# Kernel tuning notes

Hardware: AMD Instinct MI355X
Metric: run time of the kernel (lower is better)

## Reference

```python
import jax, jax.numpy as jnp
import numpy as np

B, T, N = 16, 16, 1024          # patients, max visits, code_num
C, G, H, A, P = 48, 32, 150, 32, 32  # code_size, graph_size, hidden_size, t_attention_size, pool attn size
OUT = 1
NEG = -1e30


def setup_inputs() -> dict:
    key = jax.random.key(0)
    ks = jax.random.split(key, 20)
    code_x = (jax.random.uniform(ks[0], (B, T, N)) < 0.2).astype(jnp.float32)
    neighbors = (jax.random.uniform(ks[1], (B, T, N)) < 0.2).astype(jnp.float32)
    cat = jax.random.randint(ks[2], (B, T, N), 0, 8)
    # divided[..., 0/1/2] = disjoint m1 (persistent) / m2 (emerging-neighbor) / m3 (emerging-unrelated) masks
    divided = jnp.stack([(cat == 0), (cat == 1), (cat == 2)], axis=-1).astype(jnp.int32)
    lens = jax.random.randint(ks[3], (B,), 1, T + 1)
    prior = jax.random.uniform(ks[4], (N,))
    adj = (jax.random.uniform(ks[5], (N, N)) * (jax.random.uniform(ks[6], (N, N)) < 0.05)).astype(jnp.float32)

    def nrm(k, shape, scale=0.05):
        return (jax.random.normal(k, shape) * scale).astype(jnp.float32)

    return dict(
        code_x=code_x, divided=divided, neighbors=neighbors, lens=lens, prior=prior, adj=adj,
        c_emb=nrm(ks[7], (N, C)), n_emb=nrm(ks[8], (N, C)), u_emb=nrm(ks[9], (N, G)),
        Wg=nrm(ks[10], (C, G)), bg=jnp.zeros((G,), jnp.float32),
        W_ih=nrm(ks[11], (3 * H, G)), b_ih=jnp.zeros((3 * H,), jnp.float32),
        W_hh=nrm(ks[12], (3 * H, H)), b_hh=jnp.zeros((3 * H,), jnp.float32),
        Wq=nrm(ks[13], (G, A)), bq=jnp.zeros((A,), jnp.float32),
        Wk=nrm(ks[14], (G, A)), bk=jnp.zeros((A,), jnp.float32),
        Wv=nrm(ks[15], (G, H)), bv=jnp.zeros((H,), jnp.float32),
        Wp=nrm(ks[16], (H, P)), bp=jnp.zeros((P,), jnp.float32),
        ctx=nrm(ks[17], (P,)),
        Wc=nrm(ks[18], (H, OUT)), bc=jnp.zeros((OUT,), jnp.float32),
    )


def _forward(code_x, divided, neighbors, lens, prior, adj, c_emb, n_emb, u_emb,
             Wg, bg, W_ih, b_ih, W_hh, b_hh, Wq, bq, Wk, bk, Wv, bv,
             Wp, bp, ctx, Wc, bc):
    pr = prior[:, None]                                  # [N,1] disease prior scaling of graph messages
    scale = 1.0 / jnp.sqrt(jnp.asarray(A, jnp.float32))

    def gru(x, h):
        # torch nn.GRUCell semantics; x: [B,N,G], h: [B,N,H]
        gi = jnp.einsum('bng,kg->bnk', x, W_ih) + b_ih
        gh = jnp.einsum('bnh,kh->bnk', h, W_hh) + b_hh
        ir, iz, i_n = jnp.split(gi, 3, -1)
        hr, hz, h_n = jnp.split(gh, 3, -1)
        r = jax.nn.sigmoid(ir + hr)
        z = jax.nn.sigmoid(iz + hz)
        cand = jnp.tanh(i_n + r * h_n)
        return (1.0 - z) * cand + z * h

    def step(carry, xs):
        h_prev, no_prev, t = carry
        cx, nb, dv = xs                                  # [B,N], [B,N], [B,N,3]
        c = cx[..., None]
        n = nb[..., None]
        # --- GraphLayer: adjacency message passing, prior-weighted ---
        ce = c * c_emb                                   # [B,N,C]
        ne = n * n_emb
        agg_c = jnp.einsum('mn,bnc->bmc', adj, ce) * pr
        agg_n = jnp.einsum('mn,bnc->bmc', adj, ne) * pr
        co = jax.nn.leaky_relu((ce + c * (agg_c + agg_n)) @ Wg + bg)   # [B,N,G]
        no = jax.nn.leaky_relu((ne + n * (agg_n + agg_c)) @ Wg + bg)
        # --- TransitionLayer ---
        m1 = dv[..., 0] > 0
        m2 = dv[..., 1] > 0
        m3 = dv[..., 2] > 0
        m23 = m2 | m3
        h_gru = gru(co, h_prev)                          # GRU branch for persistent codes (m1)
        # attention branch: queries = prev-step neighbor embeddings (m2) or unrelated embeddings (m3)
        qf = jnp.where(m2[..., None], no_prev, 0.0) + jnp.where(m3[..., None], u_emb, 0.0)
        q = qf @ Wq + bq
        k = co @ Wk + bk
        v = co @ Wv + bv                                 # [B,N,H]
        g = jnp.einsum('bma,bna->bmn', q, k) * scale     # scores over active m2|m3 keys only
        g = jnp.where(m23[:, None, :], g, NEG)
        h_att = jnp.tanh(jnp.einsum('bmn,bnh->bmh', jax.nn.softmax(g, axis=-1), v))
        t_pos = (t > 0).astype(co.dtype)                 # m23 branch only runs for t > 0 (as in original)
        h_new = jnp.where(m1[..., None], h_gru, 0.0) + t_pos * jnp.where(m23[..., None], h_att, 0.0)
        # masked maxes (0 when the index set is empty, as in original)
        om1 = jnp.max(jnp.where(m1[..., None], h_gru, NEG), axis=1)
        om1 = jnp.where(jnp.any(m1, axis=1)[:, None], om1, 0.0)
        om23 = jnp.max(jnp.where(m23[..., None], h_att, NEG), axis=1)
        om23 = jnp.where(jnp.any(m23, axis=1)[:, None], om23, 0.0)
        out_t = om1 + t_pos * om23                       # [B,H]
        return (h_new, no, t + 1), out_t

    h0 = jnp.zeros((B, N, H), jnp.float32)
    no0 = jnp.zeros((B, N, G), jnp.float32)
    xs = (jnp.transpose(code_x, (1, 0, 2)),
          jnp.transpose(neighbors, (1, 0, 2)),
          jnp.transpose(divided, (1, 0, 2, 3)))
    _, outs = jax.lax.scan(step, (h0, no0, jnp.int32(0)), xs)
    outs = jnp.transpose(outs, (1, 0, 2))                # [B,T,H]
    # --- DotProductAttention pooling over valid (ragged) timesteps ---
    vu = (outs @ Wp + bp) @ ctx                          # [B,T]
    valid = jnp.arange(T)[None, :] < lens[:, None]
    score = jax.nn.softmax(jnp.where(valid, vu, NEG), axis=-1)
    pooled = jnp.sum(outs * score[..., None], axis=1)    # [B,H]
    # --- Classifier (dropout identity at eval, activation=None) ---
    return pooled @ Wc + bc


def reference(code_x, divided, neighbors, lens, prior, adj, c_emb, n_emb, u_emb,
              Wg, bg, W_ih, b_ih, W_hh, b_hh, Wq, bq, Wk, bk, Wv, bv,
              Wp, bp, ctx, Wc, bc):
    return _forward(code_x, divided, neighbors, lens, prior, adj, c_emb, n_emb, u_emb,
                    Wg, bg, W_ih, b_ih, W_hh, b_hh, Wq, bq, Wk, bk, Wv, bv,
                    Wp, bp, ctx, Wc, bc)
```

## Files before the change

kernel.cpp:

```cpp
#include <hip/hip_runtime.h>

#define B_ 16
#define T_ 16
#define N_ 1024
#define C_ 48
#define G_ 32
#define H_ 150
#define A_ 32
#define P_ 32
#define H3_ 450
#define NNZ_CAP 262144
#define CAP1 256
#define CAP23 384
#define CHCAP 40960
#define DCAP 256
#define SCALE_ 0.17677669529663687f

__device__ __forceinline__ unsigned fenc(float f){
  unsigned u = __float_as_uint(f);
  return (u & 0x80000000u) ? ~u : (u | 0x80000000u);
}
__device__ __forceinline__ float fdec(unsigned e){
  unsigned u = (e & 0x80000000u) ? (e & 0x7fffffffu) : ~e;
  return __uint_as_float(u);
}
__device__ __forceinline__ float sigmf(float x){ return 1.f/(1.f+__expf(-x)); }
__device__ __forceinline__ float wmaxf(float v){
  #pragma unroll
  for (int d=32; d>0; d>>=1) v = fmaxf(v, __shfl_xor(v,d));
  return v;
}

#define FMA16(W, PTR, ACC) do { \
    const float4* _c4 = (const float4*)(PTR); \
    float4 _c0=_c4[0], _c1=_c4[1], _c2=_c4[2], _c3=_c4[3]; \
    ACC[0]=fmaf((W),_c0.x,ACC[0]); ACC[1]=fmaf((W),_c0.y,ACC[1]); \
    ACC[2]=fmaf((W),_c0.z,ACC[2]); ACC[3]=fmaf((W),_c0.w,ACC[3]); \
    ACC[4]=fmaf((W),_c1.x,ACC[4]); ACC[5]=fmaf((W),_c1.y,ACC[5]); \
    ACC[6]=fmaf((W),_c1.z,ACC[6]); ACC[7]=fmaf((W),_c1.w,ACC[7]); \
    ACC[8]=fmaf((W),_c2.x,ACC[8]); ACC[9]=fmaf((W),_c2.y,ACC[9]); \
    ACC[10]=fmaf((W),_c2.z,ACC[10]); ACC[11]=fmaf((W),_c2.w,ACC[11]); \
    ACC[12]=fmaf((W),_c3.x,ACC[12]); ACC[13]=fmaf((W),_c3.y,ACC[13]); \
    ACC[14]=fmaf((W),_c3.z,ACC[14]); ACC[15]=fmaf((W),_c3.w,ACC[15]); \
  } while(0)

__global__ void k_csr_cnt(const float* __restrict__ adj, int* __restrict__ rcnt){
  int m = blockIdx.x; int tid = threadIdx.x;
  int c = 0;
  for (int n = tid; n < N_; n += 256) c += (adj[(size_t)m*N_+n] != 0.f) ? 1 : 0;
  __shared__ int sr[256];
  sr[tid]=c; __syncthreads();
  for (int s=128; s>0; s>>=1){ if (tid<s) sr[tid]+=sr[tid+s]; __syncthreads(); }
  if (tid==0) rcnt[m]=sr[0];
}
__global__ void k_csr_scan(const int* __restrict__ rcnt, int* __restrict__ rowptr){
  int lane = threadIdx.x;
  int s = 0;
  for (int r=0;r<16;++r) s += rcnt[lane*16+r];
  int incl = s;
  for (int d=1; d<64; d<<=1){ int y = __shfl_up(incl, d); if (lane>=d) incl += y; }
  int run = incl - s;
  for (int r=0;r<16;++r){ rowptr[lane*16+r] = run; run += rcnt[lane*16+r]; }
  if (lane==63) rowptr[N_] = incl;
}
__global__ void k_csr_fill(const float* __restrict__ adj, const float* __restrict__ prior,
                           const int* __restrict__ rowptr,
                           int* __restrict__ ccol, float* __restrict__ cval){
  int m = blockIdx.x; int lane = threadIdx.x;
// ... 61 lines not shown
    if (len >= 2){ int i2 = atomicAdd(&nLv[1],1); if (i2 < 8192) chLv[i2]=enc; }
    if (len >= 3){ int i2 = atomicAdd(&nLv[2],1); if (i2 < 2048) chLv[8192+i2]=enc; }
    if (len >= 4){ int i2 = atomicAdd(&nLv[3],1); if (i2 < DCAP) chD[i2]=enc; }
  }
}

__global__ void k_wt(const float* __restrict__ W_ih, const float* __restrict__ W_hh,
                     const float* __restrict__ Wq, const float* __restrict__ bq,
                     const float* __restrict__ Wk, const float* __restrict__ Wv,
                     float* __restrict__ WihT, float* __restrict__ WhhT,
                     float* __restrict__ Md, float* __restrict__ WvT){
  int idx = blockIdx.x*256+threadIdx.x;
  if (idx < G_*H3_){ int g=idx/H3_, k=idx-g*H3_; WihT[g*H3_+k]=W_ih[(size_t)k*G_+g]; }
  int idx2 = idx - G_*H3_;
  if (idx2>=0 && idx2 < H_*H3_){ int h=idx2/H3_, k=idx2-h*H3_; WhhT[h*H3_+k]=W_hh[(size_t)k*H_+h]; }
  int e = idx - (G_*H3_ + H_*H3_);
  if (e>=0 && e<1024){
    int g=e>>5, gp=e&31;
    float acc=0.f;
    #pragma unroll
    for (int a=0;a<A_;++a) acc = fmaf(Wq[g*A_+a], Wk[gp*A_+a], acc);
    Md[e]=acc;
  }
  int e2 = e - 1024;
  if (e2>=0 && e2<32){
    float acc=0.f;
    #pragma unroll
    for (int a=0;a<A_;++a) acc = fmaf(Wk[e2*A_+a], bq[a], acc);
    Md[1024+e2]=acc;
  }
  int e3 = e - 1056;
  if (e3>=0 && e3 < H_*G_){
    int h = e3>>5, g = e3&31;
    WvT[e3] = Wv[(size_t)g*H_+h];
  }
}

__global__ void k_init(float* __restrict__ om23f, int* __restrict__ nchN,
                       int* __restrict__ nchH, int* __restrict__ nLv){
  int i = blockIdx.x*256+threadIdx.x;
  if (i<B_*T_*H_){ om23f[i]=0.f; }
  if (i==0){ *nchN = 0; *nchH = 0; }
  if (i<16) nLv[i]=0;
}

__global__ __launch_bounds__(256) void k_cono(
    const float* __restrict__ code_x, const float* __restrict__ neighbors,
    const int* __restrict__ divided,
    const int* __restrict__ rowptr, const int* __restrict__ ccol, const float* __restrict__ cval,
    const float* __restrict__ c_emb, const float* __restrict__ n_emb,
    const float* __restrict__ Wg, const float* __restrict__ bg,
    float* __restrict__ co, float* __restrict__ no_)
{
  __shared__ float sCo[4][C_], sNo[4][C_];
  int w = threadIdx.x >> 6, lane = threadIdx.x & 63;
  int gw = blockIdx.x*4 + w;
  int bt = gw >> 10, m = gw & (N_-1);
  int t = bt & (T_-1);
  const int* dv = &divided[(size_t)gw*3];
  int d0=dv[0], d1=dv[1], d2=dv[2];
  bool needCo = (d0|d1|d2) > 0;
  bool needNo = (t < T_-1) && (divided[((size_t)(gw+N_))*3+1] > 0);
  if (!needCo && !needNo) return;
  float cxm = code_x[gw], nbm = neighbors[gw];
  float acc = 0.f;
  bool needAcc = (needCo && cxm!=0.f) || (needNo && nbm!=0.f);
  if (needAcc){
    int s = rowptr[m], e = rowptr[m+1];
    if (s > NNZ_CAP) s = NNZ_CAP;
    if (e > NNZ_CAP) e = NNZ_CAP;
    int btN = bt << 10;
    for (int base = s; base < e; base += 64){
      int j = base + lane;
      int cc = 0; float wx = 0.f, wy = 0.f;
      if (j < e){
        cc = ccol[j];
        float cv = cval[j];
        float xs = code_x[btN+cc], ys = neighbors[btN+cc];
        wx = cv*xs; wy = cv*ys;
      }
      unsigned long long mk = __ballot(wx!=0.f || wy!=0.f);
      while (mk){
        int u0 = __builtin_ctzll(mk); mk &= (mk-1ULL);
        int u1 = -1;
        if (mk){ u1 = __builtin_ctzll(mk); mk &= (mk-1ULL); }
        int u1s = (u1>=0)? u1 : u0;
        int n0 = __shfl(cc,u0); float a0x=__shfl(wx,u0), a0y=__shfl(wy,u0);
        int n1 = __shfl(cc,u1s); float a1x=__shfl(wx,u1s), a1y=__shfl(wy,u1s);
        float ce0=0.f,ne0=0.f,ce1=0.f,ne1=0.f;
        if (lane < C_){
          ce0 = c_emb[(size_t)n0*C_+lane]; ne0 = n_emb[(size_t)n0*C_+lane];
          ce1 = c_emb[(size_t)n1*C_+lane]; ne1 = n_emb[(size_t)n1*C_+lane];
        }
        acc = fmaf(a0x, ce0, acc); acc = fmaf(a0y, ne0, acc);
        if (u1>=0){ acc = fmaf(a1x, ce1, acc); acc = fmaf(a1y, ne1, acc); }
      }
    }
  }
  if (lane < C_){
    sCo[w][lane] = cxm * (c_emb[(size_t)m*C_+lane] + acc);
    sNo[w][lane] = nbm * (n_emb[(size_t)m*C_+lane] + acc);
  }
  asm volatile("s_waitcnt lgkmcnt(0)" ::: "memory");
  int g = lane & 31; bool isNo = lane >= 32;
  const float* src = isNo ? sNo[w] : sCo[w];
  float a2 = bg[g];
  #pragma unroll
  for (int c=0;c<C_;++c) a2 = fmaf(src[c], Wg[c*G_+g], a2);
  float r = a2 >= 0.f ? a2 : 0.01f*a2;
  if (isNo ? needNo : needCo){
    float* dst = isNo ? no_ : co;
    dst[(size_t)gw*G_ + g] = r;
  }
}

__global__ __launch_bounds__(768) void k_attnP(
    const float* __restrict__ co, const float* __restrict__ no_,
    const float* __restrict__ u_emb, const int* __restrict__ divided,
    const int* __restrict__ lst23, const int* __restrict__ cnt23,
    const float* __restrict__ Md,
    float* __restrict__ pbH, float* __restrict__ lH)
{
  int b = blockIdx.x; int t = blockIdx.y + 1; int bt = b*T_ + t;
  int z = blockIdx.z;
  int idx = b*(T_-1) + (t-1);
  int cnt = cnt23[bt]; if (cnt > CAP23) cnt = CAP23;
  if (cnt == 0) return;
  int tid = threadIdx.x;
  int grp = (tid >= 384) ? 1 : 0;
  int r   = tid - 384*grp;
  float* pbOut = &pbH[(size_t)(z*B_*(T_-1) + idx)*CAP23*G_];
  float* lOut  = &lH[(size_t)(z*B_*(T_-1) + idx)*CAP23];
  int half = (cnt+1)>>1;
  int cs = z*half;
  int ce = cs + half; if (ce > cnt) ce = cnt;
  int hc = ce - cs;
  if (hc <= 0){
    if (tid < cnt){
      for (int j=0;j<G_;++j) pbOut[(size_t)tid*G_+j]=0.f;
      lOut[tid]=0.f;
    }
    return;
  }
  __shared__ int sLstH[192];
  __shared__ __align__(16) float sCo[192][G_];
  __shared__ float sPb[CAP23][G_];
  __shared__ float sL[CAP23];
  for (int i=tid; i<hc; i+=768) sLstH[i] = lst23[(size_t)bt*N_ + cs + i];
  __syncthreads();
  for (int i=tid; i<hc*8; i+=768){
    int c = i>>3, seg = i&7;
    float4 v = *(const float4*)&co[((((size_t)bt<<10) + sLstH[c])<<5) + seg*4];
    *(float4*)&sCo[c][seg*4] = v;
  }
  bool act = (r < cnt);
  float qpp[G_];
  if (act){
    int n = lst23[(size_t)bt*N_ + r];
    int d1 = divided[((size_t)bt*N_+n)*3+1];
    const float* qsrc = (d1>0) ? &no_[((((size_t)(bt-1))<<10)+n)<<5] : &u_emb[(size_t)n*G_];
    float4 qv[8];
    #pragma unroll
    for (int j=0;j<8;++j) qv[j] = ((const float4*)qsrc)[j];
    #pragma unroll
    for (int j=0;j<G_;++j) qpp[j] = Md[1024+j];
    #pragma unroll
    for (int g=0; g<G_; ++g){
      float qfg = (g&3)==0 ? qv[g>>2].x : (g&3)==1 ? qv[g>>2].y : (g&3)==2 ? qv[g>>2].z : qv[g>>2].w;
      const float4* mr = (const float4*)&Md[g*G_];
      #pragma unroll
      for (int j=0;j<8;++j){
        float4 mj = mr[j];
        qpp[4*j+0] = fmaf(qfg, mj.x, qpp[4*j+0]);
        qpp[4*j+1] = fmaf(qfg, mj.y, qpp[4*j+1]);
        qpp[4*j+2] = fmaf(qfg, mj.z, qpp[4*j+2]);
        qpp[4*j+3] = fmaf(qfg, mj.w, qpp[4*j+3]);
      }
    }
  } else {
    #pragma unroll
    for (int j=0;j<G_;++j) qpp[j]=0.f;
  }
  __syncthreads();
  int hh = (hc+1)>>1;
  int c0 = grp ? hh : 0;
  int c1 = grp ? hc : hh;
  float pbar[G_]; float l = 0.f;
  #pragma unroll
  for (int j=0;j<G_;++j) pbar[j]=0.f;
  if (act){
    #pragma unroll 2
    for (int c=c0;c<c1;++c){
      const float4* col = (const float4*)&sCo[c][0];
      float4 xv[8];
      #pragma unroll
      for (int j=0;j<8;++j) xv[j]=col[j];
      float d0=0.f,d1v=0.f,d2v=0.f,d3=0.f;
      #pragma unroll
      for (int j=0;j<8;j+=4){
        d0 = fmaf(qpp[4*j+0], xv[j].x, d0); d1v = fmaf(qpp[4*j+1], xv[j].y, d1v);
        d2v = fmaf(qpp[4*j+2], xv[j].z, d2v); d3 = fmaf(qpp[4*j+3], xv[j].w, d3);
        d0 = fmaf(qpp[4*j+4], xv[j+1].x, d0); d1v = fmaf(qpp[4*j+5], xv[j+1].y, d1v);
        d2v = fmaf(qpp[4*j+6], xv[j+1].z, d2v); d3 = fmaf(qpp[4*j+7], xv[j+1].w, d3);
        d0 = fmaf(qpp[4*j+8], xv[j+2].x, d0); d1v = fmaf(qpp[4*j+9], xv[j+2].y, d1v);
        d2v = fmaf(qpp[4*j+10], xv[j+2].z, d2v); d3 = fmaf(qpp[4*j+11], xv[j+2].w, d3);
        d0 = fmaf(qpp[4*j+12], xv[j+3].x, d0); d1v = fmaf(qpp[4*j+13], xv[j+3].y, d1v);
        d2v = fmaf(qpp[4*j+14], xv[j+3].z, d2v); d3 = fmaf(qpp[4*j+15], xv[j+3].w, d3);
      }
      float dot = (d0+d1v)+(d2v+d3);
      float pv = __expf(dot*SCALE_);
      l += pv;
      #pragma unroll
      for (int j=0;j<8;++j){
        pbar[4*j+0] = fmaf(pv, xv[j].x, pbar[4*j+0]);
        pbar[4*j+1] = fmaf(pv, xv[j].y, pbar[4*j+1]);
        pbar[4*j+2] = fmaf(pv, xv[j].z, pbar[4*j+2]);
        pbar[4*j+3] = fmaf(pv, xv[j].w, pbar[4*j+3]);
      }
    }
  }
  __syncthreads();
  if (act && grp==0){
    #pragma unroll
    for (int j=0;j<G_;++j) sPb[r][(j+r)&31] = pbar[j];
    sL[r] = l;
  }
  __syncthreads();
  if (act && grp==1){
    #pragma unroll
    for (int j=0;j<G_;++j) sPb[r][(j+r)&31] += pbar[j];
    sL[r] += l;
  }
  __syncthreads();
  for (int i=tid; i<cnt*G_; i+=768){
    int rr = i>>5, j = i&31;
    pbOut[(size_t)rr*G_ + j] = sPb[rr][(j+rr)&31];
  }
  for (int i=tid; i<cnt; i+=768) lOut[i] = sL[i];
}

__global__ __launch_bounds__(768) void k_attnC(
    const int* __restrict__ divided, const int* __restrict__ lst23,
    const int* __restrict__ cnt23, const int* __restrict__ pos1,
    const float* __restrict__ WvT, const float* __restrict__ bv,
    const float* __restrict__ pbH, const float* __restrict__ lH,
    float* __restrict__ hsel, float* __restrict__ om23f)
{
  int b = blockIdx.x; int t = blockIdx.y + 1; int bt = b*T_ + t;
  int idx = b*(T_-1) + (t-1);
  int cnt = cnt23[bt]; if (cnt > CAP23) cnt = CAP23;
  if (cnt == 0) return;
  __shared__ unsigned sMax[H_];
  int tid = threadIdx.x;
  int grp = (tid >= 384) ? 1 : 0;
  int r   = tid - 384*grp;
  int lane = tid & 63;
  unsigned sent = fenc(-1e30f);
  for (int i=tid; i<H_; i+=768) sMax[i] = sent;
  __syncthreads();
  bool act = (r < cnt);
  float pb[G_];
  if (act){
    const float4* p0 = (const float4*)&pbH[((size_t)(0*B_*(T_-1) + idx)*CAP23 + r)*G_];
    const float4* p1 = (const float4*)&pbH[((size_t)(1*B_*(T_-1) + idx)*CAP23 + r)*G_];
    float l = lH[(size_t)(0*B_*(T_-1)+idx)*CAP23 + r] + lH[(size_t)(1*B_*(T_-1)+idx)*CAP23 + r];
    float inv = 1.f/l;
    #pragma unroll
    for (int j=0;j<8;++j){
      float4 a = p0[j], c = p1[j];
      pb[4*j+0]=(a.x+c.x)*inv; pb[4*j+1]=(a.y+c.y)*inv;
      pb[4*j+2]=(a.z+c.z)*inv; pb[4*j+3]=(a.w+c.w)*inv;
    }
  } else {
    #pragma unroll
    for (int j=0;j<G_;++j) pb[j]=0.f;
  }
  bool wsel=false; float* hd=nullptr;
  if (act && t+1 < T_){
    int n = lst23[(size_t)bt*N_ + r];
    size_t nidx = ((size_t)b*T_+(t+1))*N_ + n;
    if (divided[nidx*3+0] > 0){
      int pos = pos1[nidx];
      if (pos >= 0 && pos < CAP1){ wsel=true; hd=&hsel[(((size_t)b*T_+t)*CAP1 + pos)*H_]; }
    }
  }
  int hA = grp*75, hB = hA + 75;
  for (int h=hA; h<hB; ++h){
    float acc = bv[h];
    const float4* wr = (const float4*)&WvT[h*G_];
    #pragma unroll
    for (int j=0;j<8;++j){
      float4 wj = wr[j];
      acc = fmaf(pb[4*j+0], wj.x, acc);
      acc = fmaf(pb[4*j+1], wj.y, acc);
      acc = fmaf(pb[4*j+2], wj.z, acc);
      acc = fmaf(pb[4*j+3], wj.w, acc);
    }
    float o = act ? tanhf(acc) : -1e30f;
    float om = wmaxf(o);
    if (lane==0) atomicMax(&sMax[h], fenc(om));
    if (wsel) hd[h] = o;
  }
  __syncthreads();
  for (int i=tid; i<H_; i+=768) om23f[(size_t)bt*H_+i] = fdec(sMax[i]);
}

__global__ __launch_bounds__(256) void k_gruheadN(
    const float* __restrict__ co, const int* __restrict__ pos1,
    const unsigned* __restrict__ chN, const int* __restrict__ nchN,
    const float* __restrict__ WihT, const float* __restrict__ b_ih,
    const float* __restrict__ b_hh, float* __restrict__ gout)
{
  __shared__ __align__(16) float sCoT[G_][16];
  __shared__ float sG[16][452];
  __shared__ int sBt[16], sN[16], sPos[16];
  int tid = threadIdx.x;
  int NC = *nchN; if (NC > CHCAP) NC = CHCAP;
  int base = blockIdx.x * 16;
  if (base >= NC) return;
  int num = min(16, NC - base);
  if (tid < 16){
    if (tid < num){
      unsigned cl = chN[base+tid];
      int b = cl>>18, n = (cl>>8)&1023, t0 = (cl>>4)&15;
      int bt = b*T_ + t0;
      sBt[tid]=bt; sN[tid]=n; sPos[tid]=pos1[(size_t)bt*N_+n];
    } else { sBt[tid]=0; sN[tid]=0; sPos[tid]=-1; }
  }
  __syncthreads();
  for (int i=tid; i<G_*16; i+=256){
    int g = i>>4, ii = i&15;
    sCoT[g][ii] = (ii<num) ? co[((size_t)sBt[ii]*N_+sN[ii])*G_+g] : 0.f;
  }
  __syncthreads();
  for (int pass=0; pass<2; ++pass){
    int k = pass*256 + tid;
    if (k < H3_){
      float acc[16];
      #pragma unroll
      for (int u=0;u<16;++u) acc[u]=0.f;
      for (int g=0; g<G_; ++g){
        float wih = WihT[g*H3_ + k];
        FMA16(wih, &sCoT[g][0], acc);
      }
      #pragma unroll
      for (int u=0;u<16;++u) sG[u][k] = acc[u];
    }
  }
  __syncthreads();
  for (int i=tid; i<num*152; i+=256){
    int s = i/152, h = i - s*152;
    if (h < H_){
      int pos = sPos[s];
      if (pos >= 0 && pos < CAP1){
        float r = sigmf(sG[s][h]       + b_ih[h]       + b_hh[h]);
        float z = sigmf(sG[s][h+H_]    + b_ih[h+H_]    + b_hh[h+H_]);
        float cand = tanhf(sG[s][h+2*H_] + b_ih[h+2*H_] + r*b_hh[h+2*H_]);
// ... 369 lines not shown

extern "C" void kernel_launch(void* const* d_in, const int* in_sizes, int n_in,
                              void* d_out, int out_size, void* d_ws, size_t ws_size,
                              hipStream_t stream)
{
  const float* code_x=(const float*)d_in[0];
  const int*   divided=(const int*)d_in[1];
  const float* neighbors=(const float*)d_in[2];
  const int*   lens=(const int*)d_in[3];
  const float* prior=(const float*)d_in[4];
  const float* adj=(const float*)d_in[5];
  const float* c_emb=(const float*)d_in[6];
  const float* n_emb=(const float*)d_in[7];
  const float* u_emb=(const float*)d_in[8];
  const float* Wg=(const float*)d_in[9];
  const float* bg=(const float*)d_in[10];
  const float* W_ih=(const float*)d_in[11];
  const float* b_ih=(const float*)d_in[12];
  const float* W_hh=(const float*)d_in[13];
  const float* b_hh=(const float*)d_in[14];
  const float* Wq=(const float*)d_in[15];
  const float* bq=(const float*)d_in[16];
  const float* Wk=(const float*)d_in[17];
  const float* bk=(const float*)d_in[18];
  const float* Wv=(const float*)d_in[19];
  const float* bv=(const float*)d_in[20];
  const float* Wp=(const float*)d_in[21];
  const float* bp=(const float*)d_in[22];
  const float* ctx=(const float*)d_in[23];
  const float* Wc=(const float*)d_in[24];
  const float* bc=(const float*)d_in[25];
  float* out=(float*)d_out;
  (void)in_sizes; (void)n_in; (void)out_size; (void)ws_size; (void)bk;

  char* p=(char*)d_ws;
  size_t off=0;
  auto carve=[&](size_t bytes)->char*{ char* r=p+off; off=(off+bytes+255)&~(size_t)255; return r; };
  int*   rowptr=(int*)carve((N_+1)*4);
  int*   rcnt  =(int*)carve(N_*4);
  int*   ccol  =(int*)carve((size_t)NNZ_CAP*4);
  float* cval  =(float*)carve((size_t)NNZ_CAP*4);
  int*   cnt23 =(int*)carve(B_*T_*4);
  int*   cnt1  =(int*)carve(B_*T_*4);
  int*   lst23 =(int*)carve((size_t)B_*T_*N_*4);
  int*   pos1  =(int*)carve((size_t)B_*T_*N_*4);
  float* co    =(float*)carve((size_t)B_*T_*N_*G_*4);
  float* no_   =(float*)carve((size_t)B_*T_*N_*G_*4);
  float* WihT  =(float*)carve((size_t)G_*H3_*4);
  float* WhhT  =(float*)carve((size_t)H_*H3_*4);
  float* Md    =(float*)carve(1056*4);
  float* WvT   =(float*)carve((size_t)H_*G_*4);
  float* hsel  =(float*)carve((size_t)B_*T_*CAP1*H_*4);
  float* gout  =(float*)carve((size_t)B_*T_*CAP1*H_*4);
  float* pbH   =(float*)carve((size_t)2*B_*(T_-1)*CAP23*G_*4);
  float* lH    =(float*)carve((size_t)2*B_*(T_-1)*CAP23*4);
  unsigned* chainsN=(unsigned*)carve((size_t)CHCAP*4);
  unsigned* chainsH=(unsigned*)carve((size_t)CHCAP*4);
  unsigned* chLv  =(unsigned*)carve((size_t)10240*4);
  unsigned* chD   =(unsigned*)carve((size_t)DCAP*4);
  int*   nchN  =(int*)carve(256);
  int*   nchH  =(int*)carve(256);
  int*   nLv   =(int*)carve(256);
  float* om1f  =(float*)carve((size_t)B_*T_*H_*4);
  float* om23f =(float*)carve((size_t)B_*T_*H_*4);

  k_csr_cnt<<<N_,256,0,stream>>>(adj, rcnt);
  k_csr_scan<<<1,64,0,stream>>>(rcnt, rowptr);
  k_csr_fill<<<N_,64,0,stream>>>(adj, prior, rowptr, ccol, cval);
  k_masks<<<B_*T_,64,0,stream>>>(divided, lst23, pos1, cnt23, cnt1);
  k_wt<<<343,256,0,stream>>>(W_ih, W_hh, Wq, bq, Wk, Wv, WihT, WhhT, Md, WvT);
  k_init<<<(B_*T_*H_+255)/256,256,0,stream>>>(om23f, nchN, nchH, nLv);
  k_chains<<<(B_*N_+255)/256,256,0,stream>>>(divided, chainsN, nchN, chainsH, nchH, chLv, nLv, chD);
  k_cono<<<B_*T_*N_/4,256,0,stream>>>(code_x, neighbors, divided, rowptr, ccol, cval,
                                      c_emb, n_emb, Wg, bg, co, no_);
  k_attnP<<<dim3(B_, T_-1, 2),768,0,stream>>>(co, no_, u_emb, divided,
                                      lst23, cnt23, Md, pbH, lH);
  k_attnC<<<dim3(B_, T_-1),768,0,stream>>>(divided, lst23, cnt23, pos1,
                                      WvT, bv, pbH, lH, hsel, om23f);
  k_gruheadN<<<CHCAP/16,256,0,stream>>>(co, pos1, chainsN, nchN,
                                      WihT, b_ih, b_hh, gout);
  k_gruheadH<<<CHCAP/16,256,0,stream>>>(co, hsel, pos1, chainsH, nchH,
                                      WihT, b_ih, WhhT, b_hh, gout);
  k_grulev<<<512,256,0,stream>>>(co, pos1, chLv, nLv+1,
                                      WihT, b_ih, WhhT, b_hh, gout, 1, 8192);
  k_grulev<<<128,256,0,stream>>>(co, pos1, chLv+8192, nLv+2,
                                      WihT, b_ih, WhhT, b_hh, gout, 2, 2048);
  k_grudeep<<<DCAP/16,256,0,stream>>>(co, pos1, chD, nLv+3,
                                      WihT, b_ih, WhhT, b_hh, gout);
  k_om1<<<B_*T_,256,0,stream>>>(gout, cnt1, om1f);
  k_final<<<B_,256,0,stream>>>(om1f, om23f, Wp,bp,ctx,Wc,bc, lens, out);
}
```

Before: 517.0 us.

## Parallelize CSR neighbor gather by edge groups and split query projection kernel

The graph-message gather in k_cono now spreads eight edges at a time across lane groups, with each lane covering six embedding channels. Partial sums are combined with cross-lane shuffles, replacing the serialized ballot/shuffle loop that handled one or two edges at a time. The query projection (q·Md) moves out of k_attnP into a new k_qpp kernel so that both z-halves no longer recompute it. k_attnP also stops reducing its two thread-group partials through shared memory and writes four partial slots that k_attnC sums, which removes the shared-memory buffer and its barriers at the cost of an extra launch and more global traffic.

```diff
diff --git a/kernel.cpp b/kernel.cpp
--- a/kernel.cpp
+++ b/kernel.cpp
@@ -14,6 +14,7 @@
 #define CAP23 384
 #define CHCAP 40960
 #define DCAP 256
+#define NBT_ (B_*(T_-1))
 #define SCALE_ 0.17677669529663687f
 
 __device__ __forceinline__ unsigned fenc(float f){
@@ -181,7 +182,7 @@
     const float* __restrict__ Wg, const float* __restrict__ bg,
     float* __restrict__ co, float* __restrict__ no_)
 {
-  __shared__ float sCo[4][C_], sNo[4][C_];
+  __shared__ float sCo[4][C_], sNo[4][C_], sAcc[4][C_];
   int w = threadIdx.x >> 6, lane = threadIdx.x & 63;
   int gw = blockIdx.x*4 + w;
   int bt = gw >> 10, m = gw & (N_-1);
@@ -192,43 +193,55 @@
   bool needNo = (t < T_-1) && (divided[((size_t)(gw+N_))*3+1] > 0);
   if (!needCo && !needNo) return;
   float cxm = code_x[gw], nbm = neighbors[gw];
-  float acc = 0.f;
   bool needAcc = (needCo && cxm!=0.f) || (needNo && nbm!=0.f);
+  int e8 = lane >> 3;
+  int cg = lane & 7;
   if (needAcc){
     int s = rowptr[m], e = rowptr[m+1];
     if (s > NNZ_CAP) s = NNZ_CAP;
     if (e > NNZ_CAP) e = NNZ_CAP;
     int btN = bt << 10;
-    for (int base = s; base < e; base += 64){
-      int j = base + lane;
-      int cc = 0; float wx = 0.f, wy = 0.f;
+    float a6[6] = {0.f,0.f,0.f,0.f,0.f,0.f};
+    for (int base = s; base < e; base += 8){
+      int j = base + e8;
+      int n2 = 0; float av = 0.f, xs = 0.f, ys = 0.f;
       if (j < e){
-        cc = ccol[j];
-        float cv = cval[j];
-        float xs = code_x[btN+cc], ys = neighbors[btN+cc];
-        wx = cv*xs; wy = cv*ys;
-      }
-      unsigned long long mk = __ballot(wx!=0.f || wy!=0.f);
-      while (mk){
-        int u0 = __builtin_ctzll(mk); mk &= (mk-1ULL);
-        int u1 = -1;
-        if (mk){ u1 = __builtin_ctzll(mk); mk &= (mk-1ULL); }
-        int u1s = (u1>=0)? u1 : u0;
-        int n0 = __shfl(cc,u0); float a0x=__shfl(wx,u0), a0y=__shfl(wy,u0);
-        int n1 = __shfl(cc,u1s); float a1x=__shfl(wx,u1s), a1y=__shfl(wy,u1s);
-        float ce0=0.f,ne0=0.f,ce1=0.f,ne1=0.f;
-        if (lane < C_){
-          ce0 = c_emb[(size_t)n0*C_+lane]; ne0 = n_emb[(size_t)n0*C_+lane];
-          ce1 = c_emb[(size_t)n1*C_+lane]; ne1 = n_emb[(size_t)n1*C_+lane];
+        n2 = ccol[j]; av = cval[j];
+        xs = code_x[btN+n2]; ys = neighbors[btN+n2];
+      }
+      if (xs != 0.f || ys != 0.f){
+        const float* ce = &c_emb[(size_t)n2*C_ + cg*6];
+        const float* ne = &n_emb[(size_t)n2*C_ + cg*6];
+        #pragma unroll
+        for (int k=0;k<6;++k){
+          float ev = fmaf(xs, ce[k], ys*ne[k]);
+          a6[k] = fmaf(av, ev, a6[k]);
         }
-        acc = fmaf(a0x, ce0, acc); acc = fmaf(a0y, ne0, acc);
-        if (u1>=0){ acc = fmaf(a1x, ce1, acc); acc = fmaf(a1y, ne1, acc); }
-      }
-    }
-  }
+      }
+    }
+    #pragma unroll
+    for (int k=0;k<6;++k){
+      float v = a6[k];
+      v += __shfl_xor(v, 8);
+      v += __shfl_xor(v, 16);
+      v += __shfl_xor(v, 32);
+      a6[k] = v;
+    }
+    if (lane < 8){
+      #pragma unroll
+      for (int k=0;k<6;++k) sAcc[w][lane*6+k] = a6[k];
+    }
+  } else {
+    if (lane < 8){
+      #pragma unroll
+      for (int k=0;k<6;++k) sAcc[w][lane*6+k] = 0.f;
+    }
+  }
+  asm volatile("s_waitcnt lgkmcnt(0)" ::: "memory");
+  float accv = (lane < C_) ? sAcc[w][lane] : 0.f;
   if (lane < C_){
-    sCo[w][lane] = cxm * (c_emb[(size_t)m*C_+lane] + acc);
-    sNo[w][lane] = nbm * (n_emb[(size_t)m*C_+lane] + acc);
+    sCo[w][lane] = cxm * (c_emb[(size_t)m*C_+lane] + accv);
+    sNo[w][lane] = nbm * (n_emb[(size_t)m*C_+lane] + accv);
   }
   asm volatile("s_waitcnt lgkmcnt(0)" ::: "memory");
   int g = lane & 31; bool isNo = lane >= 32;
@@ -243,11 +256,51 @@
   }
 }
 
+__global__ __launch_bounds__(256) void k_qpp(
+    const float* __restrict__ no_, const float* __restrict__ u_emb,
+    const int* __restrict__ divided, const int* __restrict__ lst23,
+    const int* __restrict__ cnt23, const float* __restrict__ Md,
+    float* __restrict__ qppB)
+{
+  int b = blockIdx.x; int t = blockIdx.y + 1; int bt = b*T_ + t;
+  int idx = b*(T_-1) + (t-1);
+  int cnt = cnt23[bt]; if (cnt > CAP23) cnt = CAP23;
+  __shared__ float sM[1056];
+  int tid = threadIdx.x;
+  for (int i=tid; i<1056; i+=256) sM[i] = Md[i];
+  __syncthreads();
+  for (int r=tid; r<cnt; r+=256){
+    int n = lst23[(size_t)bt*N_+r];
+    int d1 = divided[((size_t)bt*N_+n)*3+1];
+    const float* qsrc = (d1>0) ? &no_[((((size_t)(bt-1))<<10)+n)<<5] : &u_emb[(size_t)n*G_];
+    float4 qv[8];
+    #pragma unroll
+    for (int j=0;j<8;++j) qv[j] = ((const float4*)qsrc)[j];
+    float qpp[G_];
+    #pragma unroll
+    for (int j=0;j<G_;++j) qpp[j] = sM[1024+j];
+    #pragma unroll
+    for (int g=0; g<G_; ++g){
+      float qfg = (g&3)==0 ? qv[g>>2].x : (g&3)==1 ? qv[g>>2].y : (g&3)==2 ? qv[g>>2].z : qv[g>>2].w;
+      const float4* mr = (const float4*)&sM[g*G_];
+      #pragma unroll
+      for (int j=0;j<8;++j){
+        float4 mj = mr[j];
+        qpp[4*j+0] = fmaf(qfg, mj.x, qpp[4*j+0]);
+        qpp[4*j+1] = fmaf(qfg, mj.y, qpp[4*j+1]);
+        qpp[4*j+2] = fmaf(qfg, mj.z, qpp[4*j+2]);
+        qpp[4*j+3] = fmaf(qfg, mj.w, qpp[4*j+3]);
+      }
+    }
+    float4* po = (float4*)&qppB[((size_t)idx*CAP23 + r)*G_];
+    #pragma unroll
+    for (int j=0;j<8;++j) po[j] = make_float4(qpp[4*j+0],qpp[4*j+1],qpp[4*j+2],qpp[4*j+3]);
+  }
+}
+
 __global__ __launch_bounds__(768) void k_attnP(
-    const float* __restrict__ co, const float* __restrict__ no_,
-    const float* __restrict__ u_emb, const int* __restrict__ divided,
-    const int* __restrict__ lst23, const int* __restrict__ cnt23,
-    const float* __restrict__ Md,
+    const float* __restrict__ co, const int* __restrict__ lst23,
+    const int* __restrict__ cnt23, const float* __restrict__ qppB,
     float* __restrict__ pbH, float* __restrict__ lH)
 {
   int b = blockIdx.x; int t = blockIdx.y + 1; int bt = b*T_ + t;
@@ -258,23 +311,12 @@
   int tid = threadIdx.x;
   int grp = (tid >= 384) ? 1 : 0;
   int r   = tid - 384*grp;
-  float* pbOut = &pbH[(size_t)(z*B_*(T_-1) + idx)*CAP23*G_];
-  float* lOut  = &lH[(size_t)(z*B_*(T_-1) + idx)*CAP23];
+  __shared__ int sLstH[192];
+  __shared__ __align__(16) float sCo[192][G_];
   int half = (cnt+1)>>1;
   int cs = z*half;
   int ce = cs + half; if (ce > cnt) ce = cnt;
-  int hc = ce - cs;
-  if (hc <= 0){
-    if (tid < cnt){
-      for (int j=0;j<G_;++j) pbOut[(size_t)tid*G_+j]=0.f;
-      lOut[tid]=0.f;
-    }
-    return;
-  }
-  __shared__ int sLstH[192];
-  __shared__ __align__(16) float sCo[192][G_];
-  __shared__ float sPb[CAP23][G_];
-  __shared__ float sL[CAP23];
+  int hc = ce - cs; if (hc < 0) hc = 0;
   for (int i=tid; i<hc; i+=768) sLstH[i] = lst23[(size_t)bt*N_ + cs + i];
   __syncthreads();
   for (int i=tid; i<hc*8; i+=768){
@@ -285,26 +327,11 @@
   bool act = (r < cnt);
   float qpp[G_];
   if (act){
-    int n = lst23[(size_t)bt*N_ + r];
-    int d1 = divided[((size_t)bt*N_+n)*3+1];
-    const float* qsrc = (d1>0) ? &no_[((((size_t)(bt-1))<<10)+n)<<5] : &u_emb[(size_t)n*G_];
-    float4 qv[8];
-    #pragma unroll
-    for (int j=0;j<8;++j) qv[j] = ((const float4*)qsrc)[j];
-    #pragma unroll
-    for (int j=0;j<G_;++j) qpp[j] = Md[1024+j];
-    #pragma unroll
-    for (int g=0; g<G_; ++g){
-      float qfg = (g&3)==0 ? qv[g>>2].x : (g&3)==1 ? qv[g>>2].y : (g&3)==2 ? qv[g>>2].z : qv[g>>2].w;
-      const float4* mr = (const float4*)&Md[g*G_];
-      #pragma unroll
-      for (int j=0;j<8;++j){
-        float4 mj = mr[j];
-        qpp[4*j+0] = fmaf(qfg, mj.x, qpp[4*j+0]);
-        qpp[4*j+1] = fmaf(qfg, mj.y, qpp[4*j+1]);
-        qpp[4*j+2] = fmaf(qfg, mj.z, qpp[4*j+2]);
-        qpp[4*j+3] = fmaf(qfg, mj.w, qpp[4*j+3]);
-      }
+    const float4* qr = (const float4*)&qppB[((size_t)idx*CAP23 + r)*G_];
+    #pragma unroll
+    for (int j=0;j<8;++j){
+      float4 q = qr[j];
+      qpp[4*j+0]=q.x; qpp[4*j+1]=q.y; qpp[4*j+2]=q.z; qpp[4*j+3]=q.w;
     }
   } else {
     #pragma unroll
@@ -348,24 +375,13 @@
       }
     }
   }
-  __syncthreads();
-  if (act && grp==0){
-    #pragma unroll
-    for (int j=0;j<G_;++j) sPb[r][(j+r)&31] = pbar[j];
-    sL[r] = l;
-  }
-  __syncthreads();
-  if (act && grp==1){
-    #pragma unroll
-    for (int j=0;j<G_;++j) sPb[r][(j+r)&31] += pbar[j];
-    sL[r] += l;
-  }
-  __syncthreads();
-  for (int i=tid; i<cnt*G_; i+=768){
-    int rr = i>>5, j = i&31;
-    pbOut[(size_t)rr*G_ + j] = sPb[rr][(j+rr)&31];
-  }
-  for (int i=tid; i<cnt; i+=768) lOut[i] = sL[i];
+  if (act){
+    int slot = z*2 + grp;
+    float4* po = (float4*)&pbH[((size_t)(slot*NBT_ + idx)*CAP23 + r)*G_];
+    #pragma unroll
+    for (int j=0;j<8;++j) po[j] = make_float4(pbar[4*j+0],pbar[4*j+1],pbar[4*j+2],pbar[4*j+3]);
+    lH[(size_t)(slot*NBT_ + idx)*CAP23 + r] = l;
+  }
 }
 
 __global__ __launch_bounds__(768) void k_attnC(
@@ -390,15 +406,18 @@
   bool act = (r < cnt);
   float pb[G_];
   if (act){
-    const float4* p0 = (const float4*)&pbH[((size_t)(0*B_*(T_-1) + idx)*CAP23 + r)*G_];
-    const float4* p1 = (const float4*)&pbH[((size_t)(1*B_*(T_-1) + idx)*CAP23 + r)*G_];
-    float l = lH[(size_t)(0*B_*(T_-1)+idx)*CAP23 + r] + lH[(size_t)(1*B_*(T_-1)+idx)*CAP23 + r];
+    const float4* p0 = (const float4*)&pbH[((size_t)(0*NBT_ + idx)*CAP23 + r)*G_];
+    const float4* p1 = (const float4*)&pbH[((size_t)(1*NBT_ + idx)*CAP23 + r)*G_];
+    const float4* p2 = (const float4*)&pbH[((size_t)(2*NBT_ + idx)*CAP23 + r)*G_];
+    const float4* p3 = (const float4*)&pbH[((size_t)(3*NBT_ + idx)*CAP23 + r)*G_];
+    float l = lH[(size_t)(0*NBT_+idx)*CAP23 + r] + lH[(size_t)(1*NBT_+idx)*CAP23 + r]
+            + lH[(size_t)(2*NBT_+idx)*CAP23 + r] + lH[(size_t)(3*NBT_+idx)*CAP23 + r];
     float inv = 1.f/l;
     #pragma unroll
     for (int j=0;j<8;++j){
-      float4 a = p0[j], c = p1[j];
-      pb[4*j+0]=(a.x+c.x)*inv; pb[4*j+1]=(a.y+c.y)*inv;
-      pb[4*j+2]=(a.z+c.z)*inv; pb[4*j+3]=(a.w+c.w)*inv;
+      float4 a = p0[j], c = p1[j], d = p2[j], e = p3[j];
+      pb[4*j+0]=((a.x+c.x)+(d.x+e.x))*inv; pb[4*j+1]=((a.y+c.y)+(d.y+e.y))*inv;
+      pb[4*j+2]=((a.z+c.z)+(d.z+e.z))*inv; pb[4*j+3]=((a.w+c.w)+(d.w+e.w))*inv;
     }
   } else {
     #pragma unroll
@@ -907,8 +926,9 @@
   float* WvT   =(float*)carve((size_t)H_*G_*4);
   float* hsel  =(float*)carve((size_t)B_*T_*CAP1*H_*4);
   float* gout  =(float*)carve((size_t)B_*T_*CAP1*H_*4);
-  float* pbH   =(float*)carve((size_t)2*B_*(T_-1)*CAP23*G_*4);
-  float* lH    =(float*)carve((size_t)2*B_*(T_-1)*CAP23*4);
+  float* qppB  =(float*)carve((size_t)NBT_*CAP23*G_*4);
+  float* pbH   =(float*)carve((size_t)4*NBT_*CAP23*G_*4);
+  float* lH    =(float*)carve((size_t)4*NBT_*CAP23*4);
   unsigned* chainsN=(unsigned*)carve((size_t)CHCAP*4);
   unsigned* chainsH=(unsigned*)carve((size_t)CHCAP*4);
   unsigned* chLv  =(unsigned*)carve((size_t)10240*4);
@@ -928,8 +948,8 @@
   k_chains<<<(B_*N_+255)/256,256,0,stream>>>(divided, chainsN, nchN, chainsH, nchH, chLv, nLv, chD);
   k_cono<<<B_*T_*N_/4,256,0,stream>>>(code_x, neighbors, divided, rowptr, ccol, cval,
                                       c_emb, n_emb, Wg, bg, co, no_);
-  k_attnP<<<dim3(B_, T_-1, 2),768,0,stream>>>(co, no_, u_emb, divided,
-                                      lst23, cnt23, Md, pbH, lH);
+  k_qpp<<<dim3(B_, T_-1),256,0,stream>>>(no_, u_emb, divided, lst23, cnt23, Md, qppB);
+  k_attnP<<<dim3(B_, T_-1, 2),768,0,stream>>>(co, lst23, cnt23, qppB, pbH, lH);
   k_attnC<<<dim3(B_, T_-1),768,0,stream>>>(divided, lst23, cnt23, pos1,
                                       WvT, bv, pbH, lH, hsel, om23f);
   k_gruheadN<<<CHCAP/16,256,0,stream>>>(co, pos1, chainsN, nchN,
```

New measurement: 531.0 us. 1.03x slower.

## Fuse attention score and value-projection kernels into one block per visit

Applied to the files above, without the earlier changes.

Merges k_attnP and k_attnC into a single k_attn kernel with 512 threads per (patient, visit) block. This removes the global pbH/lH intermediate buffers and one launch. The key split over two blocks is dropped, so each thread now handles two query rows, sharing each loaded key vector between them. Partial sums are reduced in shared memory by reusing the sCo buffer. The cost is fewer blocks (240 instead of 480 attention blocks) and more registers per thread, which may reduce parallelism and occupancy.

```diff
diff --git a/kernel.cpp b/kernel.cpp
--- a/kernel.cpp
+++ b/kernel.cpp
@@ -243,195 +243,178 @@
   }
 }
 
-__global__ __launch_bounds__(768) void k_attnP(
+__global__ __launch_bounds__(512) void k_attn(
     const float* __restrict__ co, const float* __restrict__ no_,
     const float* __restrict__ u_emb, const int* __restrict__ divided,
-    const int* __restrict__ lst23, const int* __restrict__ cnt23,
-    const float* __restrict__ Md,
-    float* __restrict__ pbH, float* __restrict__ lH)
+    const int* __restrict__ lst23, const int* __restrict__ cnt23, const int* __restrict__ pos1,
+    const float* __restrict__ Md, const float* __restrict__ WvT, const float* __restrict__ bv,
+    float* __restrict__ hsel, float* __restrict__ om23f)
 {
   int b = blockIdx.x; int t = blockIdx.y + 1; int bt = b*T_ + t;
-  int z = blockIdx.z;
-  int idx = b*(T_-1) + (t-1);
   int cnt = cnt23[bt]; if (cnt > CAP23) cnt = CAP23;
   if (cnt == 0) return;
+  __shared__ int   sLst[CAP23];
+  __shared__ __align__(16) float sCo[CAP23][G_];
+  __shared__ float sL[CAP23];
+  __shared__ unsigned sMax[H_];
   int tid = threadIdx.x;
-  int grp = (tid >= 384) ? 1 : 0;
-  int r   = tid - 384*grp;
-  float* pbOut = &pbH[(size_t)(z*B_*(T_-1) + idx)*CAP23*G_];
-  float* lOut  = &lH[(size_t)(z*B_*(T_-1) + idx)*CAP23];
-  int half = (cnt+1)>>1;
-  int cs = z*half;
-  int ce = cs + half; if (ce > cnt) ce = cnt;
-  int hc = ce - cs;
-  if (hc <= 0){
-    if (tid < cnt){
-      for (int j=0;j<G_;++j) pbOut[(size_t)tid*G_+j]=0.f;
-      lOut[tid]=0.f;
-    }
-    return;
-  }
-  __shared__ int sLstH[192];
-  __shared__ __align__(16) float sCo[192][G_];
-  __shared__ float sPb[CAP23][G_];
-  __shared__ float sL[CAP23];
-  for (int i=tid; i<hc; i+=768) sLstH[i] = lst23[(size_t)bt*N_ + cs + i];
-  __syncthreads();
-  for (int i=tid; i<hc*8; i+=768){
-    int c = i>>3, seg = i&7;
-    float4 v = *(const float4*)&co[((((size_t)bt<<10) + sLstH[c])<<5) + seg*4];
-    *(float4*)&sCo[c][seg*4] = v;
-  }
-  bool act = (r < cnt);
-  float qpp[G_];
-  if (act){
-    int n = lst23[(size_t)bt*N_ + r];
-    int d1 = divided[((size_t)bt*N_+n)*3+1];
-    const float* qsrc = (d1>0) ? &no_[((((size_t)(bt-1))<<10)+n)<<5] : &u_emb[(size_t)n*G_];
-    float4 qv[8];
+  int grp = tid >> 8;
+  int rr  = tid & 255;
+  unsigned sent = fenc(-1e30f);
+  for (int i=tid; i<cnt; i+=512) sLst[i] = lst23[(size_t)bt*N_+i];
+  for (int i=tid; i<H_; i+=512) sMax[i] = sent;
+  __syncthreads();
+  for (int i=tid; i<cnt*8; i+=512){
+    int rrow = i>>3, seg = i&7;
+    float4 v = *(const float4*)&co[((((size_t)bt<<10) + sLst[rrow])<<5) + seg*4];
+    *(float4*)&sCo[rrow][seg*4] = v;
+  }
+  int r0 = 2*rr, r1 = 2*rr+1;
+  bool act0 = r0 < cnt, act1 = r1 < cnt;
+  float qpp0[G_], qpp1[G_];
+  {
+    float4 qv0[8], qv1[8];
+    if (act0){
+      int n = sLst[r0];
+      int d1 = divided[((size_t)bt*N_+n)*3+1];
+      const float* qs = (d1>0) ? &no_[((((size_t)(bt-1))<<10)+n)<<5] : &u_emb[(size_t)n*G_];
+      #pragma unroll
+      for (int j=0;j<8;++j) qv0[j] = ((const float4*)qs)[j];
+    } else {
+      #pragma unroll
+      for (int j=0;j<8;++j) qv0[j] = make_float4(0.f,0.f,0.f,0.f);
+    }
+    if (act1){
+      int n = sLst[r1];
+      int d1 = divided[((size_t)bt*N_+n)*3+1];
+      const float* qs = (d1>0) ? &no_[((((size_t)(bt-1))<<10)+n)<<5] : &u_emb[(size_t)n*G_];
+      #pragma unroll
+      for (int j=0;j<8;++j) qv1[j] = ((const float4*)qs)[j];
+    } else {
+      #pragma unroll
+      for (int j=0;j<8;++j) qv1[j] = make_float4(0.f,0.f,0.f,0.f);
+    }
     #pragma unroll
-    for (int j=0;j<8;++j) qv[j] = ((const float4*)qsrc)[j];
-    #pragma unroll
-    for (int j=0;j<G_;++j) qpp[j] = Md[1024+j];
+    for (int j=0;j<G_;++j){ float dd = Md[1024+j]; qpp0[j]=dd; qpp1[j]=dd; }
     #pragma unroll
     for (int g=0; g<G_; ++g){
-      float qfg = (g&3)==0 ? qv[g>>2].x : (g&3)==1 ? qv[g>>2].y : (g&3)==2 ? qv[g>>2].z : qv[g>>2].w;
+      float q0 = (g&3)==0 ? qv0[g>>2].x : (g&3)==1 ? qv0[g>>2].y : (g&3)==2 ? qv0[g>>2].z : qv0[g>>2].w;
+      float q1 = (g&3)==0 ? qv1[g>>2].x : (g&3)==1 ? qv1[g>>2].y : (g&3)==2 ? qv1[g>>2].z : qv1[g>>2].w;
       const float4* mr = (const float4*)&Md[g*G_];
       #pragma unroll
       for (int j=0;j<8;++j){
         float4 mj = mr[j];
-        qpp[4*j+0] = fmaf(qfg, mj.x, qpp[4*j+0]);
-        qpp[4*j+1] = fmaf(qfg, mj.y, qpp[4*j+1]);
-        qpp[4*j+2] = fmaf(qfg, mj.z, qpp[4*j+2]);
-        qpp[4*j+3] = fmaf(qfg, mj.w, qpp[4*j+3]);
-      }
-    }
-  } else {
-    #pragma unroll
-    for (int j=0;j<G_;++j) qpp[j]=0.f;
-  }
-  __syncthreads();
-  int hh = (hc+1)>>1;
-  int c0 = grp ? hh : 0;
-  int c1 = grp ? hc : hh;
-  float pbar[G_]; float l = 0.f;
+        qpp0[4*j+0]=fmaf(q0,mj.x,qpp0[4*j+0]); qpp1[4*j+0]=fmaf(q1,mj.x,qpp1[4*j+0]);
+        qpp0[4*j+1]=fmaf(q0,mj.y,qpp0[4*j+1]); qpp1[4*j+1]=fmaf(q1,mj.y,qpp1[4*j+1]);
+        qpp0[4*j+2]=fmaf(q0,mj.z,qpp0[4*j+2]); qpp1[4*j+2]=fmaf(q1,mj.z,qpp1[4*j+2]);
+        qpp0[4*j+3]=fmaf(q0,mj.w,qpp0[4*j+3]); qpp1[4*j+3]=fmaf(q1,mj.w,qpp1[4*j+3]);
+      }
+    }
+  }
+  __syncthreads();
+  int half = (cnt+1)>>1;
+  int c0 = grp ? half : 0;
+  int c1 = grp ? cnt  : half;
+  float pb0[G_], pb1[G_]; float l0=0.f, l1=0.f;
   #pragma unroll
-  for (int j=0;j<G_;++j) pbar[j]=0.f;
-  if (act){
-    #pragma unroll 2
+  for (int j=0;j<G_;++j){ pb0[j]=0.f; pb1[j]=0.f; }
+  if (act0){
     for (int c=c0;c<c1;++c){
       const float4* col = (const float4*)&sCo[c][0];
       float4 xv[8];
       #pragma unroll
       for (int j=0;j<8;++j) xv[j]=col[j];
-      float d0=0.f,d1v=0.f,d2v=0.f,d3=0.f;
-      #pragma unroll
-      for (int j=0;j<8;j+=4){
-        d0 = fmaf(qpp[4*j+0], xv[j].x, d0); d1v = fmaf(qpp[4*j+1], xv[j].y, d1v);
-        d2v = fmaf(qpp[4*j+2], xv[j].z, d2v); d3 = fmaf(qpp[4*j+3], xv[j].w, d3);
-        d0 = fmaf(qpp[4*j+4], xv[j+1].x, d0); d1v = fmaf(qpp[4*j+5], xv[j+1].y, d1v);
-        d2v = fmaf(qpp[4*j+6], xv[j+1].z, d2v); d3 = fmaf(qpp[4*j+7], xv[j+1].w, d3);
-        d0 = fmaf(qpp[4*j+8], xv[j+2].x, d0); d1v = fmaf(qpp[4*j+9], xv[j+2].y, d1v);
-        d2v = fmaf(qpp[4*j+10], xv[j+2].z, d2v); d3 = fmaf(qpp[4*j+11], xv[j+2].w, d3);
-        d0 = fmaf(qpp[4*j+12], xv[j+3].x, d0); d1v = fmaf(qpp[4*j+13], xv[j+3].y, d1v);
-        d2v = fmaf(qpp[4*j+14], xv[j+3].z, d2v); d3 = fmaf(qpp[4*j+15], xv[j+3].w, d3);
-      }
-      float dot = (d0+d1v)+(d2v+d3);
-      float pv = __expf(dot*SCALE_);
-      l += pv;
+      float dA=0.f,dB=0.f,dC=0.f,dD=0.f, eA=0.f,eB=0.f,eC=0.f,eD=0.f;
       #pragma unroll
       for (int j=0;j<8;++j){
-        pbar[4*j+0] = fmaf(pv, xv[j].x, pbar[4*j+0]);
-        pbar[4*j+1] = fmaf(pv, xv[j].y, pbar[4*j+1]);
-        pbar[4*j+2] = fmaf(pv, xv[j].z, pbar[4*j+2]);
-        pbar[4*j+3] = fmaf(pv, xv[j].w, pbar[4*j+3]);
-      }
-    }
-  }
-  __syncthreads();
-  if (act && grp==0){
-    #pragma unroll
-    for (int j=0;j<G_;++j) sPb[r][(j+r)&31] = pbar[j];
-    sL[r] = l;
-  }
-  __syncthreads();
-  if (act && grp==1){
-    #pragma unroll
-    for (int j=0;j<G_;++j) sPb[r][(j+r)&31] += pbar[j];
-    sL[r] += l;
-  }
-  __syncthreads();
-  for (int i=tid; i<cnt*G_; i+=768){
-    int rr = i>>5, j = i&31;
-    pbOut[(size_t)rr*G_ + j] = sPb[rr][(j+rr)&31];
-  }
-  for (int i=tid; i<cnt; i+=768) lOut[i] = sL[i];
-}
-
-__global__ __launch_bounds__(768) void k_attnC(
-    const int* __restrict__ divided, const int* __restrict__ lst23,
-    const int* __restrict__ cnt23, const int* __restrict__ pos1,
-    const float* __restrict__ WvT, const float* __restrict__ bv,
-    const float* __restrict__ pbH, const float* __restrict__ lH,
-    float* __restrict__ hsel, float* __restrict__ om23f)
-{
-  int b = blockIdx.x; int t = blockIdx.y + 1; int bt = b*T_ + t;
-  int idx = b*(T_-1) + (t-1);
-  int cnt = cnt23[bt]; if (cnt > CAP23) cnt = CAP23;
-  if (cnt == 0) return;
-  __shared__ unsigned sMax[H_];
-  int tid = threadIdx.x;
-  int grp = (tid >= 384) ? 1 : 0;
-  int r   = tid - 384*grp;
+        dA = fmaf(qpp0[4*j+0], xv[j].x, dA); dB = fmaf(qpp0[4*j+1], xv[j].y, dB);
+        dC = fmaf(qpp0[4*j+2], xv[j].z, dC); dD = fmaf(qpp0[4*j+3], xv[j].w, dD);
+        eA = fmaf(qpp1[4*j+0], xv[j].x, eA); eB = fmaf(qpp1[4*j+1], xv[j].y, eB);
+        eC = fmaf(qpp1[4*j+2], xv[j].z, eC); eD = fmaf(qpp1[4*j+3], xv[j].w, eD);
+      }
+      float pv0 = __expf(((dA+dB)+(dC+dD))*SCALE_);
+      float pv1 = __expf(((eA+eB)+(eC+eD))*SCALE_);
+      if (!act1) pv1 = 0.f;
+      l0 += pv0; l1 += pv1;
+      #pragma unroll
+      for (int j=0;j<8;++j){
+        pb0[4*j+0]=fmaf(pv0,xv[j].x,pb0[4*j+0]); pb1[4*j+0]=fmaf(pv1,xv[j].x,pb1[4*j+0]);
+        pb0[4*j+1]=fmaf(pv0,xv[j].y,pb0[4*j+1]); pb1[4*j+1]=fmaf(pv1,xv[j].y,pb1[4*j+1]);
+        pb0[4*j+2]=fmaf(pv0,xv[j].z,pb0[4*j+2]); pb1[4*j+2]=fmaf(pv1,xv[j].z,pb1[4*j+2]);
+        pb0[4*j+3]=fmaf(pv0,xv[j].w,pb0[4*j+3]); pb1[4*j+3]=fmaf(pv1,xv[j].w,pb1[4*j+3]);
+      }
+    }
+  }
+  __syncthreads();
+  if (grp==0){
+    if (act0){
+      #pragma unroll
+      for (int j=0;j<G_;++j) sCo[r0][(j+r0)&31] = pb0[j];
+      sL[r0] = l0;
+    }
+    if (act1){
+      #pragma unroll
+      for (int j=0;j<G_;++j) sCo[r1][(j+r1)&31] = pb1[j];
+      sL[r1] = l1;
+    }
+  }
+  __syncthreads();
+  if (grp==1){
+    if (act0){
+      #pragma unroll
+      for (int j=0;j<G_;++j) sCo[r0][(j+r0)&31] += pb0[j];
+      sL[r0] += l0;
+    }
+    if (act1){
+      #pragma unroll
+      for (int j=0;j<G_;++j) sCo[r1][(j+r1)&31] += pb1[j];
+      sL[r1] += l1;
+    }
+  }
+  __syncthreads();
+  int grp2 = tid >> 8;
   int lane = tid & 63;
-  unsigned sent = fenc(-1e30f);
-  for (int i=tid; i<H_; i+=768) sMax[i] = sent;
-  __syncthreads();
-  bool act = (r < cnt);
-  float pb[G_];
-  if (act){
-    const float4* p0 = (const float4*)&pbH[((size_t)(0*B_*(T_-1) + idx)*CAP23 + r)*G_];
-    const float4* p1 = (const float4*)&pbH[((size_t)(1*B_*(T_-1) + idx)*CAP23 + r)*G_];
-    float l = lH[(size_t)(0*B_*(T_-1)+idx)*CAP23 + r] + lH[(size_t)(1*B_*(T_-1)+idx)*CAP23 + r];
-    float inv = 1.f/l;
-    #pragma unroll
-    for (int j=0;j<8;++j){
-      float4 a = p0[j], c = p1[j];
-      pb[4*j+0]=(a.x+c.x)*inv; pb[4*j+1]=(a.y+c.y)*inv;
-      pb[4*j+2]=(a.z+c.z)*inv; pb[4*j+3]=(a.w+c.w)*inv;
-    }
-  } else {
-    #pragma unroll
-    for (int j=0;j<G_;++j) pb[j]=0.f;
-  }
-  bool wsel=false; float* hd=nullptr;
-  if (act && t+1 < T_){
-    int n = lst23[(size_t)bt*N_ + r];
-    size_t nidx = ((size_t)b*T_+(t+1))*N_ + n;
-    if (divided[nidx*3+0] > 0){
-      int pos = pos1[nidx];
-      if (pos >= 0 && pos < CAP1){ wsel=true; hd=&hsel[(((size_t)b*T_+t)*CAP1 + pos)*H_]; }
-    }
-  }
-  int hA = grp*75, hB = hA + 75;
-  for (int h=hA; h<hB; ++h){
-    float acc = bv[h];
-    const float4* wr = (const float4*)&WvT[h*G_];
-    #pragma unroll
-    for (int j=0;j<8;++j){
-      float4 wj = wr[j];
-      acc = fmaf(pb[4*j+0], wj.x, acc);
-      acc = fmaf(pb[4*j+1], wj.y, acc);
-      acc = fmaf(pb[4*j+2], wj.z, acc);
-      acc = fmaf(pb[4*j+3], wj.w, acc);
-    }
-    float o = act ? tanhf(acc) : -1e30f;
-    float om = wmaxf(o);
-    if (lane==0) atomicMax(&sMax[h], fenc(om));
-    if (wsel) hd[h] = o;
-  }
-  __syncthreads();
-  for (int i=tid; i<H_; i+=768) om23f[(size_t)bt*H_+i] = fdec(sMax[i]);
+  int hA = grp2*75, hB = hA + 75;
+  for (int er = tid & 255; er < CAP23; er += 256){
+    bool act = er < cnt;
+    float pb[G_];
+    if (act){
+      float inv = 1.f / sL[er];
+      #pragma unroll
+      for (int j=0;j<G_;++j) pb[j] = sCo[er][(j+er)&31] * inv;
+    } else {
+      #pragma unroll
+      for (int j=0;j<G_;++j) pb[j]=0.f;
+    }
+    bool wsel=false; float* hd=nullptr;
+    if (act && t+1 < T_){
+      int n = sLst[er];
+      size_t nidx = ((size_t)b*T_+(t+1))*N_ + n;
+      if (divided[nidx*3+0] > 0){
+        int pos = pos1[nidx];
+        if (pos >= 0 && pos < CAP1){ wsel=true; hd=&hsel[(((size_t)b*T_+t)*CAP1 + pos)*H_]; }
+      }
+    }
+    for (int h=hA; h<hB; ++h){
+      float acc = bv[h];
+      const float4* wr = (const float4*)&WvT[h*G_];
+      #pragma unroll
+      for (int j=0;j<8;++j){
+        float4 wj = wr[j];
+        acc = fmaf(pb[4*j+0], wj.x, acc);
+        acc = fmaf(pb[4*j+1], wj.y, acc);
+        acc = fmaf(pb[4*j+2], wj.z, acc);
+        acc = fmaf(pb[4*j+3], wj.w, acc);
+      }
+      float o = act ? tanhf(acc) : -1e30f;
+      float om = wmaxf(o);
+      if (lane==0) atomicMax(&sMax[h], fenc(om));
+      if (wsel) hd[h] = o;
+    }
+    if (cnt <= 256) break;
+  }
+  __syncthreads();
+  for (int i=tid; i<H_; i+=512) om23f[(size_t)bt*H_+i] = fdec(sMax[i]);
 }
 
 __global__ __launch_bounds__(256) void k_gruheadN(
@@ -907,8 +890,6 @@
   float* WvT   =(float*)carve((size_t)H_*G_*4);
   float* hsel  =(float*)carve((size_t)B_*T_*CAP1*H_*4);
   float* gout  =(float*)carve((size_t)B_*T_*CAP1*H_*4);
-  float* pbH   =(float*)carve((size_t)2*B_*(T_-1)*CAP23*G_*4);
-  float* lH    =(float*)carve((size_t)2*B_*(T_-1)*CAP23*4);
   unsigned* chainsN=(unsigned*)carve((size_t)CHCAP*4);
   unsigned* chainsH=(unsigned*)carve((size_t)CHCAP*4);
   unsigned* chLv  =(unsigned*)carve((size_t)10240*4);
@@ -928,10 +909,9 @@
   k_chains<<<(B_*N_+255)/256,256,0,stream>>>(divided, chainsN, nchN, chainsH, nchH, chLv, nLv, chD);
   k_cono<<<B_*T_*N_/4,256,0,stream>>>(code_x, neighbors, divided, rowptr, ccol, cval,
                                       c_emb, n_emb, Wg, bg, co, no_);
-  k_attnP<<<dim3(B_, T_-1, 2),768,0,stream>>>(co, no_, u_emb, divided,
-                                      lst23, cnt23, Md, pbH, lH);
-  k_attnC<<<dim3(B_, T_-1),768,0,stream>>>(divided, lst23, cnt23, pos1,
-                                      WvT, bv, pbH, lH, hsel, om23f);
+  k_attn<<<dim3(B_, T_-1),512,0,stream>>>(co, no_, u_emb, divided,
+                                      lst23, cnt23, pos1, Md, WvT, bv,
+                                      hsel, om23f);
   k_gruheadN<<<CHCAP/16,256,0,stream>>>(co, pos1, chainsN, nchN,
                                       WihT, b_ih, b_hh, gout);
   k_gruheadH<<<CHCAP/16,256,0,stream>>>(co, hsel, pos1, chainsH, nchH,
```

New measurement: 530.6 us. +2.6%, slower.
